# Performance work log

Hardware: AMD Instinct MI355X
Metric: run time of the kernel (lower is better)

The kernel has to match this reference:

```python
import jax, jax.numpy as jnp
import numpy as np

N_PTS = 16384
DIM = 3

def setup_inputs() -> dict:
    key = jax.random.key(0)
    k1, k2 = jax.random.split(key)
    source_cloud = jax.random.normal(k1, (1, N_PTS, DIM), dtype=jnp.float32)
    target_cloud = jax.random.normal(k2, (1, N_PTS, DIM), dtype=jnp.float32)
    return {"source_cloud": source_cloud, "target_cloud": target_cloud}


def _min_sq_dists(x, y):
    # x: [B, N, D], y: [B, M, D] -> [B, N] squared distance to nearest neighbor in y
    x2 = jnp.sum(x * x, axis=-1)              # [B, N]
    y2 = jnp.sum(y * y, axis=-1)              # [B, M]
    xy = jnp.einsum('bnd,bmd->bnm', x, y)     # [B, N, M]
    d = x2[:, :, None] + y2[:, None, :] - 2.0 * xy  # squared dists, as pytorch3d knn_points
    return jnp.min(d, axis=-1)                # K=1 nearest neighbor


def reference(source_cloud, target_cloud):
    chamfer_forward = _min_sq_dists(source_cloud, target_cloud)[0]   # [N]
    chamfer_backward = _min_sq_dists(target_cloud, source_cloud)[0]  # [M]
    return (chamfer_forward, chamfer_backward)
```

## Files before the change

kernel.cpp:

```cpp
#include <hip/hip_runtime.h>

#define NPTS 16384
#define KS   16
#define BT   256
#define BROWS 256
#define TSPLIT 4
#define SWEEP (NPTS / TSPLIT)
#define NTILE (SWEEP / 32)
#define NR (NTILE / 2)

typedef __attribute__((ext_vector_type(8)))  short bf16x8;
typedef __attribute__((ext_vector_type(16))) float f32x16;
typedef __attribute__((ext_vector_type(8)))  unsigned short ushort8;

__device__ __forceinline__ unsigned short btrunc(float f) {
    return (unsigned short)(__float_as_uint(f) >> 16);
}
__device__ __forceinline__ float btruncf(float f) {
    return __uint_as_float(__float_as_uint(f) & 0xFFFF0000u);
}

__global__ void chamfer_pack(const float* __restrict__ s,
                             const float* __restrict__ t,
                             unsigned short* __restrict__ Apack,
                             unsigned short* __restrict__ Bpack,
                             float* __restrict__ sq,
                             unsigned* __restrict__ outinit)
{
    int i = blockIdx.x * blockDim.x + threadIdx.x;
    if (i >= 2 * NPTS) return;
    outinit[i] = 0x7F7F7F7Fu;
    int cloud = i >> 14;
    int p = i & (NPTS - 1);
    const float* base = cloud ? t : s;
    float x = base[3 * p], y = base[3 * p + 1], z = base[3 * p + 2];

    float xh = btruncf(x), yh = btruncf(y), zh = btruncf(z);
    float xl = x - xh, yl = y - yh, zl = z - zh;
    float q = x * x + y * y + z * z;
    float qh = btruncf(q), ql = q - qh;

    const unsigned short one = btrunc(1.0f);
    ushort8 A0 = { btrunc(-2.f * xh), btrunc(-2.f * xl), btrunc(-2.f * xh),
                   btrunc(-2.f * yh), btrunc(-2.f * yl), btrunc(-2.f * yh),
                   btrunc(-2.f * zh), btrunc(-2.f * zl) };
    ushort8 A1 = { btrunc(-2.f * zh), one, one, 0, 0, 0, 0, 0 };
    ushort8 B0 = { btrunc(xh), btrunc(xh), btrunc(xl),
                   btrunc(yh), btrunc(yh), btrunc(yl),
                   btrunc(zh), btrunc(zh) };
    ushort8 B1 = { btrunc(zl), btrunc(qh), btrunc(ql), 0, 0, 0, 0, 0 };

    *(ushort8*)(Apack + (size_t)i * KS)     = A0;
    *(ushort8*)(Apack + (size_t)i * KS + 8) = A1;
    *(ushort8*)(Bpack + (size_t)i * KS)     = B0;
    *(ushort8*)(Bpack + (size_t)i * KS + 8) = B1;
    sq[i] = q;
}

__global__ __launch_bounds__(BT, 2)
void chamfer_mfma(const unsigned short* __restrict__ Apack,
                  const unsigned short* __restrict__ Bpack,
                  const float* __restrict__ sq,
                  unsigned* __restrict__ out)
{
    const int dir = blockIdx.z;
    const unsigned short* A = Apack + (size_t)(dir ? NPTS : 0) * KS;
    const unsigned short* B = Bpack + (size_t)(dir ? 0 : NPTS) * KS;
    const float* s2 = sq + (dir ? NPTS : 0);
    unsigned* o = out + dir * NPTS;

    const int lane = threadIdx.x & 63;
    const int wv   = threadIdx.x >> 6;
    const int n32  = lane & 31;
    const int kh   = lane >> 5;

    const int rbase = blockIdx.x * BROWS + wv * 64;

    const bf16x8 a0 = *(const bf16x8*)(A + (size_t)(rbase + n32) * KS + kh * 8);
    const bf16x8 a1 = *(const bf16x8*)(A + (size_t)(rbase + 32 + n32) * KS + kh * 8);

    f32x16 mn0, mn1, zc;
#pragma unroll
    for (int r = 0; r < 16; ++r) { mn0[r] = 1e30f; mn1[r] = 1e30f; zc[r] = 0.0f; }

    const unsigned short* Bl = B + (size_t)(blockIdx.y * SWEEP + n32) * KS + kh * 8;
#define BTILE(t) (*(const bf16x8*)(Bl + (size_t)(t) * 32 * KS))

    bf16x8 b0 = BTILE(0), b1 = BTILE(1);
    bf16x8 n0 = BTILE(2), n1 = BTILE(3);

#pragma unroll 2
    for (int r = 0; r < NR; ++r) {
        int tp = (2 * r + 4 < NTILE) ? 2 * r + 4 : NTILE - 2;
        bf16x8 p0 = BTILE(tp);
        bf16x8 p1 = BTILE(tp + 1);

        f32x16 c00 = __builtin_amdgcn_mfma_f32_32x32x16_bf16(a0, b0, zc, 0, 0, 0);
        f32x16 c01 = __builtin_amdgcn_mfma_f32_32x32x16_bf16(a0, b1, zc, 0, 0, 0);
        f32x16 c10 = __builtin_amdgcn_mfma_f32_32x32x16_bf16(a1, b0, zc, 0, 0, 0);
        f32x16 c11 = __builtin_amdgcn_mfma_f32_32x32x16_bf16(a1, b1, zc, 0, 0, 0);
#pragma unroll
        for (int k = 0; k < 16; ++k)
            mn0[k] = fminf(fminf(mn0[k], c00[k]), c01[k]);
#pragma unroll
        for (int k = 0; k < 16; ++k)
            mn1[k] = fminf(fminf(mn1[k], c10[k]), c11[k]);

        b0 = n0; b1 = n1; n0 = p0; n1 = p1;
    }

#pragma unroll
    for (int r = 0; r < 16; ++r) {
        float v0 = mn0[r], v1 = mn1[r];
        v0 = fminf(v0, __shfl_xor(v0, 1, 32));  v1 = fminf(v1, __shfl_xor(v1, 1, 32));
        v0 = fminf(v0, __shfl_xor(v0, 2, 32));  v1 = fminf(v1, __shfl_xor(v1, 2, 32));
        v0 = fminf(v0, __shfl_xor(v0, 4, 32));  v1 = fminf(v1, __shfl_xor(v1, 4, 32));
        v0 = fminf(v0, __shfl_xor(v0, 8, 32));  v1 = fminf(v1, __shfl_xor(v1, 8, 32));
        v0 = fminf(v0, __shfl_xor(v0, 16, 32)); v1 = fminf(v1, __shfl_xor(v1, 16, 32));
        mn0[r] = v0; mn1[r] = v1;
    }

    if (n32 == 0) {
#pragma unroll
        for (int r = 0; r < 16; ++r) {
            int row0 = rbase + (r & 3) + 8 * (r >> 2) + 4 * kh;
            float d0 = fmaxf(mn0[r] + s2[row0], 0.0f);
            atomicMin(&o[row0], __float_as_uint(d0));
            int row1 = row0 + 32;
            float d1 = fmaxf(mn1[r] + s2[row1], 0.0f);
            atomicMin(&o[row1], __float_as_uint(d1));
        }
    }
#undef BTILE
}

extern "C" void kernel_launch(void* const* d_in, const int* in_sizes, int n_in,
                              void* d_out, int out_size, void* d_ws, size_t ws_size,
                              hipStream_t stream) {
    const float* s = (const float*)d_in[0];
    const float* t = (const float*)d_in[1];

    unsigned short* Apack = (unsigned short*)d_ws;
    unsigned short* Bpack = Apack + (size_t)2 * NPTS * KS;
    float* sq = (float*)(Bpack + (size_t)2 * NPTS * KS);

    chamfer_pack<<<(2 * NPTS + BT - 1) / BT, BT, 0, stream>>>(
        s, t, Apack, Bpack, sq, (unsigned*)d_out);

    dim3 grid(NPTS / BROWS, TSPLIT, 2);
    chamfer_mfma<<<grid, BT, 0, stream>>>(Apack, Bpack, sq, (unsigned*)d_out);
}
```

Baseline: 41.09 us.

## Stage B tiles through double-buffered LDS shared across waves

Each block now cooperatively loads 512-point chunks of the packed B cloud into a double-buffered LDS region, and every wave reads its MFMA B operands from there. Before, each wave streamed B from global memory on its own. This removes redundant global and L2 traffic across the four waves of a block. The split of the target cloud is doubled to 8 and launch bounds raised to 4 blocks per CU for more parallelism. The cost is a block barrier per chunk, 32KB of LDS per block, and twice as many atomicMin writes on the output.

```diff
diff --git a/kernel.cpp b/kernel.cpp
--- a/kernel.cpp
+++ b/kernel.cpp
@@ -4,10 +4,11 @@
 #define KS   16
 #define BT   256
 #define BROWS 256
-#define TSPLIT 4
+#define TSPLIT 8
 #define SWEEP (NPTS / TSPLIT)
-#define NTILE (SWEEP / 32)
-#define NR (NTILE / 2)
+#define CHUNK 512
+#define NCH   (SWEEP / CHUNK)
+#define CTILE (CHUNK / 32)
 
 typedef __attribute__((ext_vector_type(8)))  short bf16x8;
 typedef __attribute__((ext_vector_type(16))) float f32x16;
@@ -57,7 +58,7 @@
     sq[i] = q;
 }
 
-__global__ __launch_bounds__(BT, 2)
+__global__ __launch_bounds__(BT, 4)
 void chamfer_mfma(const unsigned short* __restrict__ Apack,
                   const unsigned short* __restrict__ Bpack,
                   const float* __restrict__ sq,
@@ -74,8 +75,9 @@
     const int n32  = lane & 31;
     const int kh   = lane >> 5;
 
+    __shared__ __align__(16) char ldsb[2][CHUNK * 32];
+
     const int rbase = blockIdx.x * BROWS + wv * 64;
-
     const bf16x8 a0 = *(const bf16x8*)(A + (size_t)(rbase + n32) * KS + kh * 8);
     const bf16x8 a1 = *(const bf16x8*)(A + (size_t)(rbase + 32 + n32) * KS + kh * 8);
 
@@ -83,41 +85,60 @@
 #pragma unroll
     for (int r = 0; r < 16; ++r) { mn0[r] = 1e30f; mn1[r] = 1e30f; zc[r] = 0.0f; }
 
-    const unsigned short* Bl = B + (size_t)(blockIdx.y * SWEEP + n32) * KS + kh * 8;
-#define BTILE(t) (*(const bf16x8*)(Bl + (size_t)(t) * 32 * KS))
+    const char* Bs = (const char*)(B + (size_t)blockIdx.y * SWEEP * KS);
+    int g0, g1, g2, g3;
+    {
+        int u0 = wv * 64 + lane;
+        g0 = ((u0)           >> 6) * 1024 + n32 * 32 + kh * 16;
+        g1 = ((u0 + 256)     >> 6) * 1024 + n32 * 32 + kh * 16;
+        g2 = ((u0 + 512)     >> 6) * 1024 + n32 * 32 + kh * 16;
+        g3 = ((u0 + 768)     >> 6) * 1024 + n32 * 32 + kh * 16;
+    }
+    const int ldsoff = (wv * 64 + lane) * 16;
 
-    bf16x8 b0 = BTILE(0), b1 = BTILE(1);
-    bf16x8 n0 = BTILE(2), n1 = BTILE(3);
+    uint4 v0, v1, v2, v3;
+#define LOADCH(ch) { const char* p = Bs + (size_t)(ch) * (CHUNK * 32);            \
+        v0 = *(const uint4*)(p + g0); v1 = *(const uint4*)(p + g1);               \
+        v2 = *(const uint4*)(p + g2); v3 = *(const uint4*)(p + g3); }
+#define WRITECH(bb) { char* q = &ldsb[bb][0] + ldsoff;                            \
+        *(uint4*)(q)         = v0; *(uint4*)(q + 4096)  = v1;                     \
+        *(uint4*)(q + 8192)  = v2; *(uint4*)(q + 12288) = v3; }
 
-#pragma unroll 2
-    for (int r = 0; r < NR; ++r) {
-        int tp = (2 * r + 4 < NTILE) ? 2 * r + 4 : NTILE - 2;
-        bf16x8 p0 = BTILE(tp);
-        bf16x8 p1 = BTILE(tp + 1);
+    LOADCH(0); WRITECH(0); LOADCH(1);
+    __syncthreads();
 
-        f32x16 c00 = __builtin_amdgcn_mfma_f32_32x32x16_bf16(a0, b0, zc, 0, 0, 0);
-        f32x16 c01 = __builtin_amdgcn_mfma_f32_32x32x16_bf16(a0, b1, zc, 0, 0, 0);
-        f32x16 c10 = __builtin_amdgcn_mfma_f32_32x32x16_bf16(a1, b0, zc, 0, 0, 0);
-        f32x16 c11 = __builtin_amdgcn_mfma_f32_32x32x16_bf16(a1, b1, zc, 0, 0, 0);
+    int cur = 0;
+    for (int ch = 0; ch < NCH; ++ch) {
+        const char* rb = &ldsb[cur][0] + kh * 512 + n32 * 16;
+#pragma unroll 4
+        for (int t = 0; t < CTILE; ++t) {
+            bf16x8 b = *(const bf16x8*)(rb + t * 1024);
+            f32x16 c0 = __builtin_amdgcn_mfma_f32_32x32x16_bf16(a0, b, zc, 0, 0, 0);
+            f32x16 c1 = __builtin_amdgcn_mfma_f32_32x32x16_bf16(a1, b, zc, 0, 0, 0);
 #pragma unroll
-        for (int k = 0; k < 16; ++k)
-            mn0[k] = fminf(fminf(mn0[k], c00[k]), c01[k]);
+            for (int k = 0; k < 16; ++k) mn0[k] = fminf(mn0[k], c0[k]);
 #pragma unroll
-        for (int k = 0; k < 16; ++k)
-            mn1[k] = fminf(fminf(mn1[k], c10[k]), c11[k]);
-
-        b0 = n0; b1 = n1; n0 = p0; n1 = p1;
+            for (int k = 0; k < 16; ++k) mn1[k] = fminf(mn1[k], c1[k]);
+        }
+        if (ch + 1 < NCH) {
+            WRITECH(cur ^ 1);
+            if (ch + 2 < NCH) LOADCH(ch + 2);
+            __syncthreads();
+        }
+        cur ^= 1;
     }
+#undef LOADCH
+#undef WRITECH
 
 #pragma unroll
     for (int r = 0; r < 16; ++r) {
-        float v0 = mn0[r], v1 = mn1[r];
-        v0 = fminf(v0, __shfl_xor(v0, 1, 32));  v1 = fminf(v1, __shfl_xor(v1, 1, 32));
-        v0 = fminf(v0, __shfl_xor(v0, 2, 32));  v1 = fminf(v1, __shfl_xor(v1, 2, 32));
-        v0 = fminf(v0, __shfl_xor(v0, 4, 32));  v1 = fminf(v1, __shfl_xor(v1, 4, 32));
-        v0 = fminf(v0, __shfl_xor(v0, 8, 32));  v1 = fminf(v1, __shfl_xor(v1, 8, 32));
-        v0 = fminf(v0, __shfl_xor(v0, 16, 32)); v1 = fminf(v1, __shfl_xor(v1, 16, 32));
-        mn0[r] = v0; mn1[r] = v1;
+        float u0 = mn0[r], u1 = mn1[r];
+        u0 = fminf(u0, __shfl_xor(u0, 1, 32));  u1 = fminf(u1, __shfl_xor(u1, 1, 32));
+        u0 = fminf(u0, __shfl_xor(u0, 2, 32));  u1 = fminf(u1, __shfl_xor(u1, 2, 32));
+        u0 = fminf(u0, __shfl_xor(u0, 4, 32));  u1 = fminf(u1, __shfl_xor(u1, 4, 32));
+        u0 = fminf(u0, __shfl_xor(u0, 8, 32));  u1 = fminf(u1, __shfl_xor(u1, 8, 32));
+        u0 = fminf(u0, __shfl_xor(u0, 16, 32)); u1 = fminf(u1, __shfl_xor(u1, 16, 32));
+        mn0[r] = u0; mn1[r] = u1;
     }
 
     if (n32 == 0) {
@@ -131,7 +152,6 @@
             atomicMin(&o[row1], __float_as_uint(d1));
         }
     }
-#undef BTILE
 }
 
 extern "C" void kernel_launch(void* const* d_in, const int* in_sizes, int n_in,
```

New measurement: 42.26 us. +2.8%, slower.

## Shrink per-wave tile to one MFMA and raise occupancy with more target splits

Applied to the files above, without the earlier changes.

Each wave now covers 32 rows with a single MFMA per target tile instead of a 2x2 register tile, and drops the manual software prefetch of B tiles. Blocks handle 128 rows and the target sweep is split 8 ways, which gives more blocks, and the launch bounds are raised to 8 blocks per SIMD-level occupancy. The aim is to hide load latency through occupancy rather than explicit prefetch and register reuse. The cost is that each B tile loaded now feeds half as many MFMAs, and there are twice as many atomicMin writes to the output.

```diff
diff --git a/kernel.cpp b/kernel.cpp
--- a/kernel.cpp
+++ b/kernel.cpp
@@ -3,11 +3,10 @@
 #define NPTS 16384
 #define KS   16
 #define BT   256
-#define BROWS 256
-#define TSPLIT 4
+#define BROWS 128
+#define TSPLIT 8
 #define SWEEP (NPTS / TSPLIT)
 #define NTILE (SWEEP / 32)
-#define NR (NTILE / 2)
 
 typedef __attribute__((ext_vector_type(8)))  short bf16x8;
 typedef __attribute__((ext_vector_type(16))) float f32x16;
@@ -57,7 +56,7 @@
     sq[i] = q;
 }
 
-__global__ __launch_bounds__(BT, 2)
+__global__ __launch_bounds__(BT, 8)
 void chamfer_mfma(const unsigned short* __restrict__ Apack,
                   const unsigned short* __restrict__ Bpack,
                   const float* __restrict__ sq,
@@ -74,64 +73,41 @@
     const int n32  = lane & 31;
     const int kh   = lane >> 5;
 
-    const int rbase = blockIdx.x * BROWS + wv * 64;
+    const int rbase = blockIdx.x * BROWS + wv * 32;
+    const bf16x8 a0 = *(const bf16x8*)(A + (size_t)(rbase + n32) * KS + kh * 8);
 
-    const bf16x8 a0 = *(const bf16x8*)(A + (size_t)(rbase + n32) * KS + kh * 8);
-    const bf16x8 a1 = *(const bf16x8*)(A + (size_t)(rbase + 32 + n32) * KS + kh * 8);
-
-    f32x16 mn0, mn1, zc;
+    f32x16 mn, zc;
 #pragma unroll
-    for (int r = 0; r < 16; ++r) { mn0[r] = 1e30f; mn1[r] = 1e30f; zc[r] = 0.0f; }
+    for (int r = 0; r < 16; ++r) { mn[r] = 1e30f; zc[r] = 0.0f; }
 
     const unsigned short* Bl = B + (size_t)(blockIdx.y * SWEEP + n32) * KS + kh * 8;
-#define BTILE(t) (*(const bf16x8*)(Bl + (size_t)(t) * 32 * KS))
 
-    bf16x8 b0 = BTILE(0), b1 = BTILE(1);
-    bf16x8 n0 = BTILE(2), n1 = BTILE(3);
-
-#pragma unroll 2
-    for (int r = 0; r < NR; ++r) {
-        int tp = (2 * r + 4 < NTILE) ? 2 * r + 4 : NTILE - 2;
-        bf16x8 p0 = BTILE(tp);
-        bf16x8 p1 = BTILE(tp + 1);
-
-        f32x16 c00 = __builtin_amdgcn_mfma_f32_32x32x16_bf16(a0, b0, zc, 0, 0, 0);
-        f32x16 c01 = __builtin_amdgcn_mfma_f32_32x32x16_bf16(a0, b1, zc, 0, 0, 0);
-        f32x16 c10 = __builtin_amdgcn_mfma_f32_32x32x16_bf16(a1, b0, zc, 0, 0, 0);
-        f32x16 c11 = __builtin_amdgcn_mfma_f32_32x32x16_bf16(a1, b1, zc, 0, 0, 0);
+    for (int t = 0; t < NTILE; ++t) {
+        bf16x8 b = *(const bf16x8*)(Bl + (size_t)t * 32 * KS);
+        f32x16 c = __builtin_amdgcn_mfma_f32_32x32x16_bf16(a0, b, zc, 0, 0, 0);
 #pragma unroll
-        for (int k = 0; k < 16; ++k)
-            mn0[k] = fminf(fminf(mn0[k], c00[k]), c01[k]);
-#pragma unroll
-        for (int k = 0; k < 16; ++k)
-            mn1[k] = fminf(fminf(mn1[k], c10[k]), c11[k]);
-
-        b0 = n0; b1 = n1; n0 = p0; n1 = p1;
+        for (int k = 0; k < 16; ++k) mn[k] = fminf(mn[k], c[k]);
     }
 
 #pragma unroll
     for (int r = 0; r < 16; ++r) {
-        float v0 = mn0[r], v1 = mn1[r];
-        v0 = fminf(v0, __shfl_xor(v0, 1, 32));  v1 = fminf(v1, __shfl_xor(v1, 1, 32));
-        v0 = fminf(v0, __shfl_xor(v0, 2, 32));  v1 = fminf(v1, __shfl_xor(v1, 2, 32));
-        v0 = fminf(v0, __shfl_xor(v0, 4, 32));  v1 = fminf(v1, __shfl_xor(v1, 4, 32));
-        v0 = fminf(v0, __shfl_xor(v0, 8, 32));  v1 = fminf(v1, __shfl_xor(v1, 8, 32));
-        v0 = fminf(v0, __shfl_xor(v0, 16, 32)); v1 = fminf(v1, __shfl_xor(v1, 16, 32));
-        mn0[r] = v0; mn1[r] = v1;
+        float v0 = mn[r];
+        v0 = fminf(v0, __shfl_xor(v0, 1, 32));
+        v0 = fminf(v0, __shfl_xor(v0, 2, 32));
+        v0 = fminf(v0, __shfl_xor(v0, 4, 32));
+        v0 = fminf(v0, __shfl_xor(v0, 8, 32));
+        v0 = fminf(v0, __shfl_xor(v0, 16, 32));
+        mn[r] = v0;
     }
 
     if (n32 == 0) {
 #pragma unroll
         for (int r = 0; r < 16; ++r) {
-            int row0 = rbase + (r & 3) + 8 * (r >> 2) + 4 * kh;
-            float d0 = fmaxf(mn0[r] + s2[row0], 0.0f);
-            atomicMin(&o[row0], __float_as_uint(d0));
-            int row1 = row0 + 32;
-            float d1 = fmaxf(mn1[r] + s2[row1], 0.0f);
-            atomicMin(&o[row1], __float_as_uint(d1));
+            int row = rbase + (r & 3) + 8 * (r >> 2) + 4 * kh;
+            float d = fmaxf(mn[r] + s2[row], 0.0f);
+            atomicMin(&o[row], __float_as_uint(d));
         }
     }
-#undef BTILE
 }
 
 extern "C" void kernel_launch(void* const* d_in, const int* in_sizes, int n_in,
```

After: 38.40 us. -6.6%, faster.
